# Kernel optimization log

Measured on AMD Instinct MI355X. Metric: run time of the kernel, lower is better.

Reference implementation:

```python
import jax, jax.numpy as jnp
import numpy as np


def setup_inputs() -> dict:
    key = jax.random.key(0)
    k1, k2 = jax.random.split(key)
    queries = jax.random.normal(k1, (8, 4096, 512), dtype=jnp.float32)
    items = jax.random.normal(k2, (1024, 512), dtype=jnp.float32)
    return {"queries": queries, "items": items}


def reference(queries, items):
    # queries: (B, S, F), items: (K, F); reduction='none', memto_framework=True
    # Phase-only (unit magnitude) reconstruction along the sequence axis.
    f = jnp.fft.rfft(queries, axis=1)                     # (B, S//2+1, F) complex64
    unit = jnp.fft.irfft(jnp.exp(-1j * jnp.angle(f)), axis=1)  # (B, S, F) float32 (S even)
    # Dense score against shared memory, then top-1 nearest memory item.
    score = jnp.einsum('bsf,kf->bsk', unit, items)        # (B, S, K)
    idx = jnp.argmax(score, axis=-1)                      # (B, S) int, top-1 index
    step_basis = items[idx]                               # gather -> (B, S, F)
    # MSE with reduction='none' is elementwise squared error; then sum over features.
    gathering_loss = jnp.sum((queries - step_basis) ** 2, axis=-1)  # (B, S)
    return gathering_loss
```

## Files before the change

kernel.cpp:

```cpp
#include <hip/hip_runtime.h>


#define NB 8
#define NS 4096
#define NF 512
#define NK 1024
#define NROWS (NB * NS)
#define NKB 8
#define KK 1024

#define SWZF(i) ((i) ^ (((i) >> 4) & 15))

typedef _Float16 half8 __attribute__((ext_vector_type(8)));
typedef float floatx4 __attribute__((ext_vector_type(4)));
struct H2 { _Float16 x, y; };

__device__ __forceinline__ float2 cmulf(float2 a, float2 b) {
    return make_float2(a.x * b.x - a.y * b.y, a.x * b.y + a.y * b.x);
}

__device__ __forceinline__ float2 unitize(float2 v) {
    float m2 = v.x * v.x + v.y * v.y;
    if (m2 > 0.f) {
        float inv = 1.0f / sqrtf(m2);
        return make_float2(v.x * inv, v.y * inv);
    }
    return make_float2(1.f, 0.f);
}

__device__ __forceinline__ H2 split_h2(float v) {
    _Float16 h = (_Float16)v;
    float lo = v - (float)h;
    H2 r; r.x = h; r.y = (_Float16)lo; return r;
}

__device__ __forceinline__ void dft4(float2 a, float2 b, float2 c, float2 d,
                                     float2& o0, float2& o1, float2& o2, float2& o3) {
    float2 apc = make_float2(a.x + c.x, a.y + c.y);
    float2 amc = make_float2(a.x - c.x, a.y - c.y);
    float2 bpd = make_float2(b.x + d.x, b.y + d.y);
    float2 bmd = make_float2(b.x - d.x, b.y - d.y);
    o0 = make_float2(apc.x + bpd.x, apc.y + bpd.y);
    o1 = make_float2(amc.x + bmd.y, amc.y - bmd.x);
    o2 = make_float2(apc.x - bpd.x, apc.y - bpd.y);
    o3 = make_float2(amc.x - bmd.y, amc.y + bmd.x);
}

__global__ void twiddle_init(float2* __restrict__ W) {
    int k = blockIdx.x * 256 + threadIdx.x;
    double ang = -2.0 * 3.14159265358979323846 * (double)k / 4096.0;
    W[k] = make_float2((float)cos(ang), (float)sin(ang));
}

__global__ __launch_bounds__(256) void transpose_kernel(
        const float* __restrict__ q, float* __restrict__ qt) {
    __shared__ float tile[32][33];
    int b = blockIdx.z;
    int s0 = blockIdx.x * 32;
    int f0 = blockIdx.y * 32;
    int tx = threadIdx.x;
    int ty = threadIdx.y;
    const float* qb = q + (size_t)b * NS * NF;
    float* qtb = qt + (size_t)b * NF * NS;
#pragma unroll
    for (int i = 0; i < 4; ++i) {
        int s = s0 + ty + i * 8;
        tile[ty + i * 8][tx] = qb[(size_t)s * NF + f0 + tx];
    }
    __syncthreads();
#pragma unroll
    for (int i = 0; i < 4; ++i) {
        int f = f0 + ty + i * 8;
        qtb[(size_t)f * NS + s0 + tx] = tile[tx][ty + i * 8];
    }
}

__device__ __forceinline__ void fft4096_r16(float2* A, float2* B,
                                            const float2* __restrict__ W, int t) {
    const float C1 = 0.92387953251128674f;
    const float S1 = 0.38268343236508978f;
    const float R2 = 0.70710678118654752f;
    const float2 w1 = make_float2(C1, -S1);
    const float2 w2 = make_float2(R2, -R2);
    const float2 w3 = make_float2(S1, -C1);
    const float2 w4 = make_float2(0.f, -1.f);
    const float2 w6 = make_float2(-R2, -R2);
    const float2 w9 = make_float2(-C1, S1);
#pragma unroll
    for (int st = 0; st < 3; ++st) {
        float2* src = (st == 1) ? B : A;
        float2* dst = (st == 1) ? A : B;
        const int s = (st == 0) ? 1 : (st == 1) ? 16 : 256;
        __syncthreads();
        float2 x[16];
#pragma unroll
        for (int j = 0; j < 16; ++j) x[j] = src[SWZF(t + j * 256)];
        float2 y[4][4];
#pragma unroll
        for (int n0 = 0; n0 < 4; ++n0)
            dft4(x[n0], x[4 + n0], x[8 + n0], x[12 + n0],
                 y[n0][0], y[n0][1], y[n0][2], y[n0][3]);
        y[1][1] = cmulf(w1, y[1][1]);
        y[1][2] = cmulf(w2, y[1][2]);
        y[1][3] = cmulf(w3, y[1][3]);
        y[2][1] = cmulf(w2, y[2][1]);
        y[2][2] = cmulf(w4, y[2][2]);
        y[2][3] = cmulf(w6, y[2][3]);
        y[3][1] = cmulf(w3, y[3][1]);
        y[3][2] = cmulf(w6, y[3][2]);
        y[3][3] = cmulf(w9, y[3][3]);
        float2 z[16];
#pragma unroll
        for (int k0 = 0; k0 < 4; ++k0)
            dft4(y[0][k0], y[1][k0], y[2][k0], y[3][k0],
                 z[k0], z[4 + k0], z[8 + k0], z[12 + k0]);
        const int q = t & (s - 1);
        const int pw = t - q;
        const int dbase = 16 * t - 15 * q;
        dst[SWZF(dbase)] = z[0];
        if (st == 2) {
#pragma unroll
            for (int j = 1; j < 16; ++j)
                dst[SWZF(dbase + j * s)] = z[j];
        } else {
#pragma unroll
            for (int j = 1; j < 16; ++j)
                dst[SWZF(dbase + j * s)] = cmulf(W[(j * pw) & 4095], z[j]);
        }
    }
}

__global__ __launch_bounds__(256) void fft_phase_kernel(
        const float* __restrict__ qt, H2* __restrict__ u2,
        const float2* __restrict__ W) {
    __shared__ float2 bufA[4096];
    __shared__ float2 bufB[4096];
    const int t = threadIdx.x;
    const float* x0 = qt + (size_t)(2 * blockIdx.x) * NS;
    const float* x1 = x0 + NS;

    const float4* a4 = (const float4*)x0;
    const float4* b4 = (const float4*)x1;
#pragma unroll
    for (int i = 0; i < 4; ++i) {
        int idx = t + i * 256;
        float4 va = a4[idx];
        float4 vb = b4[idx];
        bufA[SWZF(idx * 4 + 0)] = make_float2(va.x, vb.x);
        bufA[SWZF(idx * 4 + 1)] = make_float2(va.y, vb.y);
        bufA[SWZF(idx * 4 + 2)] = make_float2(va.z, vb.z);
        bufA[SWZF(idx * 4 + 3)] = make_float2(va.w, vb.w);
    }

    fft4096_r16(bufA, bufB, W, t);
    __syncthreads();

#pragma unroll
    for (int j = 0; j < 8; ++j) {
        int k = t + j * 256;
        if (k == 0) {
            float2 z0 = bufB[SWZF(0)];
            float2 zh = bufB[SWZF(2048)];
            float2 u00 = unitize(make_float2(z0.x, 0.f));
            float2 u10 = unitize(make_float2(z0.y, 0.f));
            bufB[SWZF(0)] = make_float2(u00.x, u10.x);
            float2 u0h = unitize(make_float2(zh.x, 0.f));
            float2 u1h = unitize(make_float2(zh.y, 0.f));
            bufB[SWZF(2048)] = make_float2(u0h.x, u1h.x);
        } else {
            float2 zk = bufB[SWZF(k)];
            float2 zm = bufB[SWZF(4096 - k)];
            float2 a = make_float2(0.5f * (zk.x + zm.x), 0.5f * (zk.y - zm.y));
            float2 bq = make_float2(0.5f * (zk.x - zm.x), 0.5f * (zk.y + zm.y));
            float2 x1k = make_float2(bq.y, -bq.x);
            float2 u0 = unitize(a);
            float2 u1 = unitize(x1k);
            bufB[SWZF(k)] = make_float2(u0.x - u1.y, u0.y + u1.x);
            bufB[SWZF(4096 - k)] = make_float2(u0.x + u1.y, u1.x - u0.y);
        }
    }

    fft4096_r16(bufB, bufA, W, t);
    __syncthreads();

    H2* o0 = u2 + (size_t)(2 * blockIdx.x) * NS;
    H2* o1 = o0 + NS;
    const float c = 0.25f;
#pragma unroll
    for (int i = 0; i < 4; ++i) {
        int idx = t + i * 256;
        H2 t0[4], t1[4];
#pragma unroll
        for (int k = 0; k < 4; ++k) {
            float2 e = bufA[SWZF(idx * 4 + k)];
            t0[k] = split_h2(e.x * c);
            t1[k] = split_h2(e.y * c);
        }
        *(float4*)&o0[idx * 4] = *(float4*)t0;
        *(float4*)&o1[idx * 4] = *(float4*)t1;
    }
}

__global__ __launch_bounds__(256) void abuild_kernel(
        const H2* __restrict__ u2, _Float16* __restrict__ a3) {
    __shared__ H2 tile[64][65];
    const int b = blockIdx.z;
    const int f0 = blockIdx.y * 64;
    const int s0 = blockIdx.x * 64;
    const int t = threadIdx.x;
    const int fr = t >> 6;
    const int sc = t & 63;
#pragma unroll
    for (int i = 0; i < 16; ++i) {
        int f = fr + i * 4;
        tile[f][sc] = u2[(size_t)(b * NF + f0 + f) * NS + s0 + sc];
    }
    __syncthreads();
    const int s = t >> 2;
    const int qd = t & 3;
    _Float16 xs[16], ys[16];
#pragma unroll
    for (int j = 0; j < 16; ++j) {
        H2 v = tile[qd * 16 + j][s];
        xs[j] = v.x;
        ys[j] = v.y;
    }
    const int f = f0 + qd * 16;
    const int s_g = b * NS + s0 + s;
    const int rb = s_g >> 4;
    const int sl = s_g & 15;
    const int kc = f >> 5;
    const int g0 = (f >> 3) & 3;
    size_t base = ((size_t)rb * 32 + kc) * 512;
    *(float4*)(a3 + base + (g0 * 16 + sl) * 8) = ((float4*)xs)[0];
    *(float4*)(a3 + base + ((g0 + 1) * 16 + sl) * 8) = ((float4*)xs)[1];
    base += 16 * 512;
    *(float4*)(a3 + base + (g0 * 16 + sl) * 8) = ((float4*)ys)[0];
    *(float4*)(a3 + base + ((g0 + 1) * 16 + sl) * 8) = ((float4*)ys)[1];
}

__global__ __launch_bounds__(256) void bbuild_kernel(
        const float* __restrict__ items, _Float16* __restrict__ b3) {
    int id = blockIdx.x * 256 + threadIdx.x;
    int n = id >> 7, fq = id & 127;
    int f = fq * 4;
    float4 v = *(const float4*)&items[(size_t)n * NF + f];
    H2 h0 = split_h2(v.x * 1024.f);
    H2 h1 = split_h2(v.y * 1024.f);
    H2 h2v = split_h2(v.z * 1024.f);
    H2 h3 = split_h2(v.w * 1024.f);
    _Float16 hs[4] = {h0.x, h1.x, h2v.x, h3.x};
    _Float16 ls[4] = {h0.y, h1.y, h2v.y, h3.y};
    const int rb = n >> 4, nl = n & 15;
    const int kc = f >> 5, g = (f >> 3) & 3, off = f & 7;
    size_t base = ((size_t)rb * 32 + kc) * 512 + (g * 16 + nl) * 8 + off;
    *(float2*)(b3 + base) = *(float2*)hs;
    *(float2*)(b3 + base + 16 * 512) = *(float2*)ls;
}

__global__ __launch_bounds__(256, 2) void gemm_mfma_argmax(
        const _Float16* __restrict__ a3, const _Float16* __restrict__ b3,
        float* __restrict__ pbest, int* __restrict__ pidx) {
    __shared__ float smemf[256];
    __shared__ int smemi[256];
    const int sb = blockIdx.x;
    const int kb = blockIdx.y;
    const int row0 = sb * 128;
    const int n0 = kb * 128;
    const int t = threadIdx.x;
    const int wid = t >> 6, l = t & 63, g = l >> 4, c = l & 15;
    const int wr = wid >> 1, wc = wid & 1;

    floatx4 acc[4][4];
#pragma unroll
    for (int m = 0; m < 4; ++m)
#pragma unroll
        for (int n = 0; n < 4; ++n) acc[m][n] = (floatx4)0.f;

    const _Float16* pa = a3 + ((size_t)(sb * 8 + wr * 4) * 32) * 512 + l * 8;
    const _Float16* pb = b3 + ((size_t)(kb * 8 + wc * 4) * 32) * 512 + l * 8;

    half8 cah[4], cal[4], cbh[4], cbl[4];
    half8 nah[4], nal[4], nbh[4], nbl[4];

#define LOADF(ah, al, bh, bl, ch)                                           \
    {                                                                       \
        _Pragma("unroll") for (int m = 0; m < 4; ++m) {                     \
            ah[m] = *(const half8*)(pa + m * 16384 + (ch) * 512);           \
            al[m] = *(const half8*)(pa + m * 16384 + (16 + (ch)) * 512);    \
        }                                                                   \
        _Pragma("unroll") for (int n = 0; n < 4; ++n) {                     \
            bh[n] = *(const half8*)(pb + n * 16384 + (ch) * 512);           \
            bl[n] = *(const half8*)(pb + n * 16384 + (16 + (ch)) * 512);    \
        }                                                                   \
    }

#define MFMAS(ah, al, bh, bl)                                               \
    {                                                                       \
        _Pragma("unroll") for (int m = 0; m < 4; ++m)                       \
        _Pragma("unroll") for (int n = 0; n < 4; ++n) {                     \
            acc[m][n] = __builtin_amdgcn_mfma_f32_16x16x32_f16(             \
                ah[m], bh[n], acc[m][n], 0, 0, 0);                          \
            acc[m][n] = __builtin_amdgcn_mfma_f32_16x16x32_f16(             \
                al[m], bh[n], acc[m][n], 0, 0, 0);                          \
            acc[m][n] = __builtin_amdgcn_mfma_f32_16x16x32_f16(             \
                ah[m], bl[n], acc[m][n], 0, 0, 0);                          \
        }                                                                   \
    }

    LOADF(cah, cal, cbh, cbl, 0);
    for (int c0 = 0; c0 < 16; c0 += 2) {
        if (c0 + 1 < 16) LOADF(nah, nal, nbh, nbl, c0 + 1);
        MFMAS(cah, cal, cbh, cbl);
        if (c0 + 2 < 16) LOADF(cah, cal, cbh, cbl, c0 + 2);
        MFMAS(nah, nal, nbh, nbl);
    }
#undef LOADF
#undef MFMAS

#pragma unroll
    for (int m = 0; m < 4; ++m) {
#pragma unroll
        for (int rr = 0; rr < 4; ++rr) {
            float best = acc[m][0][rr];
            int bi = c;
#pragma unroll
            for (int n = 1; n < 4; ++n) {
                float v = acc[m][n][rr];
                int ig = n * 16 + c;
                if (v > best) { best = v; bi = ig; }
            }
#pragma unroll
            for (int off = 1; off < 16; off <<= 1) {
                float ov = __shfl_xor(best, off);
                int oi = __shfl_xor(bi, off);
                if (ov > best || (ov == best && oi < bi)) { best = ov; bi = oi; }
            }
            if (c == 0) {
                int s_local = wr * 64 + m * 16 + 4 * g + rr;
                smemf[wc * 128 + s_local] = best;
                smemi[wc * 128 + s_local] = bi;
            }
        }
    }
    __syncthreads();
    if (t < 128) {
        float b0v = smemf[t];
        int b0i = smemi[t];
        float b1v = smemf[128 + t];
        int b1i = smemi[128 + t] + 64;
        float best = b0v; int bi = b0i;
        if (b1v > b0v) { best = b1v; bi = b1i; }
        int row = row0 + t;
        pbest[(size_t)row * NKB + kb] = best;
        pidx[(size_t)row * NKB + kb] = n0 + bi;
    }
}

__global__ __launch_bounds__(256) void combine_loss_kernel(
        const float* __restrict__ q, const float* __restrict__ items,
        const float* __restrict__ pbest, const int* __restrict__ pidx,
        float* __restrict__ out) {
    const int wid = threadIdx.x >> 6;
    const int lane = threadIdx.x & 63;
    const int row = blockIdx.x * 4 + wid;

    float best = pbest[(size_t)row * NKB];
    int bidx = pidx[(size_t)row * NKB];
#pragma unroll
    for (int g = 1; g < NKB; ++g) {
        float v = pbest[(size_t)row * NKB + g];
        if (v > best) { best = v; bidx = pidx[(size_t)row * NKB + g]; }
    }

    const float4* qr = (const float4*)(q + (size_t)row * NF);
    const float4* mr = (const float4*)(items + (size_t)bidx * NF);
    float sum = 0.f;
#pragma unroll
    for (int i = 0; i < 2; ++i) {
        float4 a = qr[lane + i * 64];
        float4 m = mr[lane + i * 64];
        float dx = a.x - m.x, dy = a.y - m.y, dz = a.z - m.z, dw = a.w - m.w;
        sum += dx * dx + dy * dy + dz * dz + dw * dw;
    }
#pragma unroll
    for (int off = 32; off; off >>= 1) sum += __shfl_down(sum, off, 64);
    if (lane == 0) out[row] = sum;
}

extern "C" void kernel_launch(void* const* d_in, const int* in_sizes, int n_in,
                              void* d_out, int out_size, void* d_ws, size_t ws_size,
                              hipStream_t stream) {
    const float* q = (const float*)d_in[0];
    const float* items = (const float*)d_in[1];
    float* out = (float*)d_out;

    char* ws = (char*)d_ws;
    float2* W = (float2*)ws;
    float* qt = (float*)(ws + 32768);
    _Float16* a3 = (_Float16*)(ws + 32768);
    H2* u2 = (H2*)(ws + 32768 + (size_t)67108864);
    _Float16* b3 = (_Float16*)(ws + 32768 + (size_t)67108864 * 2);
    float* pbest = (float*)(ws + 32768 + (size_t)67108864 * 2 + 2097152);
    int* pidx = (int*)(ws + 32768 + (size_t)67108864 * 2 + 2097152 + 1048576);

    hipLaunchKernelGGL(twiddle_init, dim3(16), dim3(256), 0, stream, W);
    hipLaunchKernelGGL(transpose_kernel, dim3(128, 16, 8), dim3(32, 8, 1), 0,
                       stream, q, qt);
    hipLaunchKernelGGL(fft_phase_kernel, dim3(2048), dim3(256), 0, stream,
                       qt, u2, W);
    hipLaunchKernelGGL(abuild_kernel, dim3(64, 8, 8), dim3(256), 0, stream,
                       u2, a3);
    hipLaunchKernelGGL(bbuild_kernel, dim3(512), dim3(256), 0, stream,
                       items, b3);
    hipLaunchKernelGGL(gemm_mfma_argmax, dim3(256, 8), dim3(256), 0, stream,
                       a3, b3, pbest, pidx);
    hipLaunchKernelGGL(combine_loss_kernel, dim3(NROWS / 4), dim3(256), 0,
                       stream, q, items, pbest, pidx, out);
}
```

Baseline: 314.2 us.

## Fuse transpose into FFT load and remap GEMM blocks per XCD

Removes the separate transpose kernel. The FFT kernel now reads two adjacent feature columns straight from the strided query tensor, as float2 loads with a stride of NF, which saves a full 64MB write and re-read of the transposed copy. The GEMM grid is flattened and block IDs are remapped so that each XCD handles a contiguous range of row blocks across all item blocks, aiming for better L2 reuse of the A tiles. The strided 8-byte loads coalesce poorly compared with the old float4 loads, so the FFT kernel's load phase may get slower.

```diff
diff --git a/kernel.cpp b/kernel.cpp
--- a/kernel.cpp
+++ b/kernel.cpp
@@ -7,7 +7,6 @@
 #define NK 1024
 #define NROWS (NB * NS)
 #define NKB 8
-#define KK 1024
 
 #define SWZF(i) ((i) ^ (((i) >> 4) & 15))
 
@@ -50,29 +49,6 @@
     int k = blockIdx.x * 256 + threadIdx.x;
     double ang = -2.0 * 3.14159265358979323846 * (double)k / 4096.0;
     W[k] = make_float2((float)cos(ang), (float)sin(ang));
-}
-
-__global__ __launch_bounds__(256) void transpose_kernel(
-        const float* __restrict__ q, float* __restrict__ qt) {
-    __shared__ float tile[32][33];
-    int b = blockIdx.z;
-    int s0 = blockIdx.x * 32;
-    int f0 = blockIdx.y * 32;
-    int tx = threadIdx.x;
-    int ty = threadIdx.y;
-    const float* qb = q + (size_t)b * NS * NF;
-    float* qtb = qt + (size_t)b * NF * NS;
-#pragma unroll
-    for (int i = 0; i < 4; ++i) {
-        int s = s0 + ty + i * 8;
-        tile[ty + i * 8][tx] = qb[(size_t)s * NF + f0 + tx];
-    }
-    __syncthreads();
-#pragma unroll
-    for (int i = 0; i < 4; ++i) {
-        int f = f0 + ty + i * 8;
-        qtb[(size_t)f * NS + s0 + tx] = tile[tx][ty + i * 8];
-    }
 }
 
 __device__ __forceinline__ void fft4096_r16(float2* A, float2* B,
@@ -131,25 +107,21 @@
 }
 
 __global__ __launch_bounds__(256) void fft_phase_kernel(
-        const float* __restrict__ qt, H2* __restrict__ u2,
+        const float* __restrict__ q, H2* __restrict__ u2,
         const float2* __restrict__ W) {
     __shared__ float2 bufA[4096];
     __shared__ float2 bufB[4096];
     const int t = threadIdx.x;
-    const float* x0 = qt + (size_t)(2 * blockIdx.x) * NS;
-    const float* x1 = x0 + NS;
-
-    const float4* a4 = (const float4*)x0;
-    const float4* b4 = (const float4*)x1;
-#pragma unroll
-    for (int i = 0; i < 4; ++i) {
-        int idx = t + i * 256;
-        float4 va = a4[idx];
-        float4 vb = b4[idx];
-        bufA[SWZF(idx * 4 + 0)] = make_float2(va.x, vb.x);
-        bufA[SWZF(idx * 4 + 1)] = make_float2(va.y, vb.y);
-        bufA[SWZF(idx * 4 + 2)] = make_float2(va.z, vb.z);
-        bufA[SWZF(idx * 4 + 3)] = make_float2(va.w, vb.w);
+    const int p = blockIdx.x;
+    const int b = p >> 8;
+    const int f0 = (p & 255) * 2;
+    const float* qb = q + (size_t)b * NS * NF + f0;
+
+#pragma unroll
+    for (int i = 0; i < 16; ++i) {
+        int s = t + i * 256;
+        float2 v = *(const float2*)&qb[(size_t)s * NF];
+        bufA[SWZF(s)] = v;
     }
 
     fft4096_r16(bufA, bufB, W, t);
@@ -183,7 +155,7 @@
     fft4096_r16(bufB, bufA, W, t);
     __syncthreads();
 
-    H2* o0 = u2 + (size_t)(2 * blockIdx.x) * NS;
+    H2* o0 = u2 + (size_t)(2 * p) * NS;
     H2* o1 = o0 + NS;
     const float c = 0.25f;
 #pragma unroll
@@ -263,8 +235,11 @@
         float* __restrict__ pbest, int* __restrict__ pidx) {
     __shared__ float smemf[256];
     __shared__ int smemi[256];
-    const int sb = blockIdx.x;
-    const int kb = blockIdx.y;
+    const int id = blockIdx.x;
+    const int xcd = id & 7;
+    const int j = id >> 3;
+    const int kb = j & 7;
+    const int sb = xcd * 32 + (j >> 3);
     const int row0 = sb * 128;
     const int n0 = kb * 128;
     const int t = threadIdx.x;
@@ -397,7 +372,6 @@
 
     char* ws = (char*)d_ws;
     float2* W = (float2*)ws;
-    float* qt = (float*)(ws + 32768);
     _Float16* a3 = (_Float16*)(ws + 32768);
     H2* u2 = (H2*)(ws + 32768 + (size_t)67108864);
     _Float16* b3 = (_Float16*)(ws + 32768 + (size_t)67108864 * 2);
@@ -405,15 +379,13 @@
     int* pidx = (int*)(ws + 32768 + (size_t)67108864 * 2 + 2097152 + 1048576);
 
     hipLaunchKernelGGL(twiddle_init, dim3(16), dim3(256), 0, stream, W);
-    hipLaunchKernelGGL(transpose_kernel, dim3(128, 16, 8), dim3(32, 8, 1), 0,
-                       stream, q, qt);
     hipLaunchKernelGGL(fft_phase_kernel, dim3(2048), dim3(256), 0, stream,
-                       qt, u2, W);
+                       q, u2, W);
     hipLaunchKernelGGL(abuild_kernel, dim3(64, 8, 8), dim3(256), 0, stream,
                        u2, a3);
     hipLaunchKernelGGL(bbuild_kernel, dim3(512), dim3(256), 0, stream,
                        items, b3);
-    hipLaunchKernelGGL(gemm_mfma_argmax, dim3(256, 8), dim3(256), 0, stream,
+    hipLaunchKernelGGL(gemm_mfma_argmax, dim3(2048), dim3(256), 0, stream,
                        a3, b3, pbest, pidx);
     hipLaunchKernelGGL(combine_loss_kernel, dim3(NROWS / 4), dim3(256), 0,
                        stream, q, items, pbest, pidx, out);
```

Result: slower. 332.0 us (+5.7%).
